# Optimization experiments

Hardware: AMD Instinct MI355X
Metric: run time of the kernel (lower is better)

## Reference

```python
import jax, jax.numpy as jnp
import numpy as np
import math

V, D, L, H, F, MAXLEN = 32000, 1024, 6, 16, 4096, 2048
B, S = 2, 2048
DK = D // H
EPS = 1e-5


def _ln(x, g, b):
    m = jnp.mean(x, axis=-1, keepdims=True)
    v = jnp.mean((x - m) ** 2, axis=-1, keepdims=True)
    return (x - m) / jnp.sqrt(v + EPS) * g + b


def setup_inputs() -> dict:
    key = jax.random.key(0)
    ks = jax.random.split(key, 12)
    std = 0.02
    inp = {
        "tokens": jax.random.randint(ks[0], (B, S), 0, V),
        "tok_emb": jax.random.normal(ks[1], (V, D), jnp.float32) * std,
        "pos_emb": jax.random.normal(ks[2], (MAXLEN, D), jnp.float32) * std,
        "Wq": jax.random.normal(ks[3], (L, D, D), jnp.float32) * std,
        "Wk": jax.random.normal(ks[4], (L, D, D), jnp.float32) * std,
        "Wv": jax.random.normal(ks[5], (L, D, D), jnp.float32) * std,
        "Wo": jax.random.normal(ks[6], (L, D, D), jnp.float32) * std,
        "ln1_g": jnp.ones((L, D), jnp.float32),
        "ln1_b": jnp.zeros((L, D), jnp.float32),
        "ln2_g": jnp.ones((L, D), jnp.float32),
        "ln2_b": jnp.zeros((L, D), jnp.float32),
        "W1": jax.random.normal(ks[7], (L, D, F), jnp.float32) * std,
        "b1": jnp.zeros((L, F), jnp.float32),
        "W2": jax.random.normal(ks[8], (L, F, D), jnp.float32) * std,
        "b2": jnp.zeros((L, D), jnp.float32),
        "lnf_g": jnp.ones((D,), jnp.float32),
        "lnf_b": jnp.zeros((D,), jnp.float32),
        "Wout": jax.random.normal(ks[9], (D, V), jnp.float32) * std,
    }
    return inp


def _block(x, Wq, Wk, Wv, Wo, ln1_g, ln1_b, ln2_g, ln2_b, W1, b1, W2, b2, mask):
    # causal multi-head attention (pre-LN)
    h = _ln(x, ln1_g, ln1_b)
    q = (h @ Wq).reshape(B, S, H, DK)
    k = (h @ Wk).reshape(B, S, H, DK)
    v = (h @ Wv).reshape(B, S, H, DK)
    scores = jnp.einsum("bqhd,bkhd->bhqk", q, k) / math.sqrt(DK)
    scores = jnp.where(mask, scores, -jnp.inf)
    attn = jax.nn.softmax(scores, axis=-1)
    ctx = jnp.einsum("bhqk,bkhd->bqhd", attn, v).reshape(B, S, D)
    x = x + ctx @ Wo
    # feed-forward
    h = _ln(x, ln2_g, ln2_b)
    h = jax.nn.gelu(h @ W1 + b1, approximate=False)
    x = x + h @ W2 + b2
    return x


def reference(tokens, tok_emb, pos_emb, Wq, Wk, Wv, Wo, ln1_g, ln1_b, ln2_g, ln2_b,
              W1, b1, W2, b2, lnf_g, lnf_b, Wout):
    x = tok_emb[tokens] + pos_emb[:S][None, :, :]  # [B,S,D]
    mask = jnp.tril(jnp.ones((S, S), bool))[None, None]  # [1,1,S,S]
    for l in range(L):
        x = _block(x, Wq[l], Wk[l], Wv[l], Wo[l], ln1_g[l], ln1_b[l],
                   ln2_g[l], ln2_b[l], W1[l], b1[l], W2[l], b2[l], mask)
    x = _ln(x, lnf_g, lnf_b)
    return x @ Wout  # [B,S,V] logits
```

## Files before the change

### kernel.cpp

```cpp
#include <hip/hip_runtime.h>
#include <stdint.h>

typedef unsigned short u16;
typedef __bf16 bf16x8 __attribute__((ext_vector_type(8)));
typedef u16   u16x8  __attribute__((ext_vector_type(8)));
typedef float f32x4  __attribute__((ext_vector_type(4)));

#define AS1(p) (const __attribute__((address_space(1))) void*)(p)
#define AS3(p) (__attribute__((address_space(3))) void*)(p)

__device__ __forceinline__ u16 f2b(float f){
  uint32_t u = __builtin_bit_cast(uint32_t, f);
  u = (u + 0x7FFFu + ((u >> 16) & 1u)) >> 16;
  return (u16)u;
}
__device__ __forceinline__ float fexp2(float x){
#if __has_builtin(__builtin_amdgcn_exp2f)
  return __builtin_amdgcn_exp2f(x);
#else
  return exp2f(x);
#endif
}

__global__ __launch_bounds__(256) void embed_k(const int* __restrict__ tokens,
                                               const float* __restrict__ te,
                                               const float* __restrict__ pe,
                                               float* __restrict__ x){
  const int n = blockIdx.x, tid = threadIdx.x;
  const int tok = tokens[n];
  float4 a = *(const float4*)&te[(size_t)tok * 1024 + tid * 4];
  const float4 p = *(const float4*)&pe[(size_t)(n & 2047) * 1024 + tid * 4];
  a.x += p.x; a.y += p.y; a.z += p.z; a.w += p.w;
  *(float4*)&x[(size_t)n * 1024 + tid * 4] = a;
}

__global__ __launch_bounds__(256) void ln_k(const float* __restrict__ x,
                                            const float* __restrict__ g,
                                            const float* __restrict__ b,
                                            u16* __restrict__ h){
  const int row = blockIdx.x, tid = threadIdx.x;
  const float4 v = *(const float4*)&x[(size_t)row * 1024 + tid * 4];
  float s = v.x + v.y + v.z + v.w;
  float q = v.x*v.x + v.y*v.y + v.z*v.z + v.w*v.w;
#pragma unroll
  for (int m = 32; m; m >>= 1){ s += __shfl_xor(s, m); q += __shfl_xor(q, m); }
  __shared__ float ss[4], qq[4];
  if ((tid & 63) == 0){ ss[tid >> 6] = s; qq[tid >> 6] = q; }
  __syncthreads();
  s = ss[0] + ss[1] + ss[2] + ss[3];
  q = qq[0] + qq[1] + qq[2] + qq[3];
  const float mean = s * (1.f/1024.f);
  const float var  = q * (1.f/1024.f) - mean*mean;
  const float rstd = rsqrtf(var + 1e-5f);
  const float4 gv = *(const float4*)&g[tid*4];
  const float4 bv = *(const float4*)&b[tid*4];
  ushort4 o;
  o.x = f2b((v.x-mean)*rstd*gv.x + bv.x);
  o.y = f2b((v.y-mean)*rstd*gv.y + bv.y);
  o.z = f2b((v.z-mean)*rstd*gv.z + bv.z);
  o.w = f2b((v.w-mean)*rstd*gv.w + bv.w);
  *(ushort4*)&h[(size_t)row * 1024 + tid * 4] = o;
}

__device__ __forceinline__ void conv_tile(const float* __restrict__ src,
                                          u16* __restrict__ dst,
                                          int R, int C, int bx, int by,
                                          u16 (*t)[72], int tid){
  const int r0 = by * 64, c0 = bx * 64;
  const int row = tid >> 4, col4 = tid & 15;
#pragma unroll
  for (int p = 0; p < 4; ++p){
    const int r = row + p * 16;
    const float4 v = *(const float4*)&src[(size_t)(r0 + r) * C + c0 + col4 * 4];
    t[r][col4*4+0] = f2b(v.x); t[r][col4*4+1] = f2b(v.y);
    t[r][col4*4+2] = f2b(v.z); t[r][col4*4+3] = f2b(v.w);
  }
  __syncthreads();
#pragma unroll
  for (int p = 0; p < 4; ++p){
    const int rr = row + p * 16;
    ushort4 w;
    w.x = t[col4*4+0][rr]; w.y = t[col4*4+1][rr];
    w.z = t[col4*4+2][rr]; w.w = t[col4*4+3][rr];
    *(ushort4*)&dst[(size_t)(c0 + rr) * R + r0 + col4 * 4] = w;
  }
}

__global__ __launch_bounds__(256) void conv_t(const float* __restrict__ src,
                                              u16* __restrict__ dst,
                                              int R, int C){
  __shared__ u16 t[64][72];
  conv_tile(src, dst, R, C, blockIdx.x, blockIdx.y, t, threadIdx.x);
}

__global__ __launch_bounds__(256) void conv6_k(const float* __restrict__ Wq,
                                               const float* __restrict__ Wk,
                                               const float* __restrict__ Wv,
                                               const float* __restrict__ Wo,
                                               const float* __restrict__ W1,
                                               const float* __restrict__ W2,
                                               u16* __restrict__ qkvT,
                                               u16* __restrict__ woT,
                                               u16* __restrict__ w1T,
                                               u16* __restrict__ w2T){
  __shared__ u16 t[64][72];
  const int id = blockIdx.x;
  const float* src; u16* dst; int R, C, bx, by;
  if (id < 1024){
    R = 1024; C = 1024;
    const int m = id >> 8, tt = id & 255; bx = tt & 15; by = tt >> 4;
    if (m == 0){ src = Wq; dst = qkvT; }
    else if (m == 1){ src = Wk; dst = qkvT + 1048576; }
    else if (m == 2){ src = Wv; dst = qkvT + 2097152; }
    else { src = Wo; dst = woT; }
  } else if (id < 2048){
    const int tt = id - 1024; R = 1024; C = 4096; bx = tt & 63; by = tt >> 6;
    src = W1; dst = w1T;
  } else {
    const int tt = id - 2048; R = 4096; C = 1024; bx = tt & 15; by = tt >> 4;
    src = W2; dst = w2T;
  }
  conv_tile(src, dst, R, C, bx, by, t, threadIdx.x);
}

template<int EPI>
__global__ __launch_bounds__(256) void gemm_bt(const u16* __restrict__ A,
                                               const u16* __restrict__ BT,
                                               void* __restrict__ Cout,
                                               const float* __restrict__ bias,
                                               int M, int N, int K){
  __shared__ __attribute__((aligned(16))) u16 As[128 * 64];
  __shared__ __attribute__((aligned(16))) u16 Bs[128 * 64];
  const int tid = threadIdx.x;
  const int lane = tid & 63, wave = tid >> 6;
  const int m0 = blockIdx.x * 128, n0 = blockIdx.y * 128;
  const int wm = wave >> 1, wn = wave & 1;
  const int l15 = lane & 15, l4 = lane >> 4;

  const int srow = tid >> 3;
  const int skb  = ((tid & 7) ^ (srow & 7)) * 8;
  const u16* Ag = A  + (size_t)(m0 + srow) * K + skb;
  const u16* Bg = BT + (size_t)(n0 + srow) * K + skb;
  char* AsB = (char*)As + wave * 1024;
  char* BsB = (char*)Bs + wave * 1024;

  f32x4 acc[4][4] = {};

  for (int k0 = 0; k0 < K; k0 += 64){
    __syncthreads();
#pragma unroll
    for (int c = 0; c < 4; ++c){
      __builtin_amdgcn_global_load_lds(AS1(Ag + (size_t)(c*32)*K + k0), AS3(AsB + c*4096), 16, 0, 0);
      __builtin_amdgcn_global_load_lds(AS1(Bg + (size_t)(c*32)*K + k0), AS3(BsB + c*4096), 16, 0, 0);
    }
    __syncthreads();
#pragma unroll
    for (int kk = 0; kk < 64; kk += 32){
      const int krd = kk + l4 * 8;
      const int kx  = (lane & 7) * 8;
      bf16x8 af[4], bfv[4];
#pragma unroll
      for (int mi = 0; mi < 4; ++mi){
        const int r = wm*64 + mi*16 + l15;
        af[mi] = *(const bf16x8*)&As[r*64 + (krd ^ kx)];
      }
#pragma unroll
      for (int ni = 0; ni < 4; ++ni){
        const int r = wn*64 + ni*16 + l15;
        bfv[ni] = *(const bf16x8*)&Bs[r*64 + (krd ^ kx)];
      }
#pragma unroll
      for (int mi = 0; mi < 4; ++mi)
#pragma unroll
        for (int ni = 0; ni < 4; ++ni)
          acc[mi][ni] = __builtin_amdgcn_mfma_f32_16x16x32_bf16(af[mi], bfv[ni], acc[mi][ni], 0, 0, 0);
    }
  }

#pragma unroll
  for (int mi = 0; mi < 4; ++mi){
    const int r = m0 + wm*64 + mi*16 + l4*4;
#pragma unroll
    for (int ni = 0; ni < 4; ++ni){
      const int c = n0 + wn*64 + ni*16 + l15;
      const f32x4 a = acc[mi][ni];
      if constexpr (EPI == 0){
        u16* C = (u16*)Cout;
#pragma unroll
        for (int j = 0; j < 4; ++j) C[(size_t)(r+j)*N + c] = f2b(a[j]);
      } else if constexpr (EPI == 1){
        float* C = (float*)Cout;
        const float bb = bias ? bias[c] : 0.f;
#pragma unroll
        for (int j = 0; j < 4; ++j){ const size_t o = (size_t)(r+j)*N + c; C[o] += a[j] + bb; }
      } else if constexpr (EPI == 2){
        u16* C = (u16*)Cout;
        const float bb = bias[c];
#pragma unroll
        for (int j = 0; j < 4; ++j){
          const float xv = a[j] + bb;
          C[(size_t)(r+j)*N + c] = f2b(0.5f * xv * (1.f + erff(xv * 0.70710678118654752f)));
        }
      } else {
        float* C = (float*)Cout;
#pragma unroll
        for (int j = 0; j < 4; ++j) C[(size_t)(r+j)*N + c] = a[j];
      }
    }
  }
}

template<int EPI>
__global__ __launch_bounds__(512) void gemm_bt2(const u16* __restrict__ A,
                                                const u16* __restrict__ BT,
                                                void* __restrict__ Cout,
                                                const float* __restrict__ bias,
                                                int M, int N, int K){
  __shared__ __attribute__((aligned(16))) u16 Ls[3][2][256*32];
  const int tid = threadIdx.x;
  const int lane = tid & 63, wave = tid >> 6;
  const int m0 = blockIdx.x * 256, n0 = blockIdx.y * 256;
  const int wm = wave >> 2, wn = wave & 3;
  const int l15 = lane & 15, l4 = lane >> 4;

  const int su  = (lane >> 3) & 7;
  const int c8  = (lane & 7) ^ su;
  const int rloc= ((lane >> 3) << 1) | (c8 >> 2);
  const int xl  = (c8 & 3) * 8;

  const u16* Asrc = A  + (size_t)(m0 + wave*16 + rloc) * K + xl;
  const u16* Bsrc = BT + (size_t)(n0 + wave*16 + rloc) * K + xl;
  char* lds0 = (char*)&Ls[0][0][0];
  const int wb = wave * 1024;

#define LOFF(r) (((r) >> 1)*64 + (((((((r) & 1) << 2) | l4)) ^ (((r) >> 1) & 7))*8))

#define STG(sb, k0, L) do{ \
    __builtin_amdgcn_global_load_lds(AS1(Asrc + (size_t)((L)*128)*K + (size_t)(k0)), \
        AS3(lds0 + (sb)*32768 +         (L)*8192 + wb), 16, 0, 0); \
    __builtin_amdgcn_global_load_lds(AS1(Bsrc + (size_t)((L)*128)*K + (size_t)(k0)), \
        AS3(lds0 + (sb)*32768 + 16384 + (L)*8192 + wb), 16, 0, 0); \
  }while(0)

#define MM(mi, a) do{ \
    acc[mi][0] = __builtin_amdgcn_mfma_f32_16x16x32_bf16((a), bf[0], acc[mi][0], 0, 0, 0); \
    acc[mi][1] = __builtin_amdgcn_mfma_f32_16x16x32_bf16((a), bf[1], acc[mi][1], 0, 0, 0); \
    acc[mi][2] = __builtin_amdgcn_mfma_f32_16x16x32_bf16((a), bf[2], acc[mi][2], 0, 0, 0); \
    acc[mi][3] = __builtin_amdgcn_mfma_f32_16x16x32_bf16((a), bf[3], acc[mi][3], 0, 0, 0); \
  }while(0)

  f32x4 acc[8][4] = {};
  const int nt = K >> 5;

  STG(0, 0, 0);  STG(0, 0, 1);
  STG(1, 32, 0); STG(1, 32, 1);
  asm volatile("s_waitcnt vmcnt(4)" ::: "memory");
  __builtin_amdgcn_s_barrier();

  int buf = 0;
  for (int t = 0; t < nt; ++t){
    const u16* LA = &Ls[buf][0][0];
    const u16* LB = &Ls[buf][1][0];
    int sb = buf + 2; if (sb >= 3) sb -= 3;
    const int kn = (t + 2) << 5;
    const bool st = (t + 2) < nt;

    bf16x8 bf[4], af0, af1;
#pragma unroll
    for (int ni = 0; ni < 4; ++ni)
      bf[ni] = *(const bf16x8*)&LB[LOFF(wn*64 + ni*16 + l15)];
    af0 = *(const bf16x8*)&LA[LOFF(wm*128 + 0*16 + l15)];
    af1 = *(const bf16x8*)&LA[LOFF(wm*128 + 1*16 + l15)];
    if (st) STG(sb, kn, 0);
    __builtin_amdgcn_s_barrier();
    __builtin_amdgcn_s_setprio(1);
    MM(0, af0); MM(1, af1);
    __builtin_amdgcn_s_setprio(0);

    af0 = *(const bf16x8*)&LA[LOFF(wm*128 + 2*16 + l15)];
    af1 = *(const bf16x8*)&LA[LOFF(wm*128 + 3*16 + l15)];
    __builtin_amdgcn_s_barrier();
    __builtin_amdgcn_s_setprio(1);
    MM(2, af0); MM(3, af1);
    __builtin_amdgcn_s_setprio(0);

    af0 = *(const bf16x8*)&LA[LOFF(wm*128 + 4*16 + l15)];
    af1 = *(const bf16x8*)&LA[LOFF(wm*128 + 5*16 + l15)];
    if (st) STG(sb, kn, 1);
    __builtin_amdgcn_s_barrier();
    __builtin_amdgcn_s_setprio(1);
    MM(4, af0); MM(5, af1);
    __builtin_amdgcn_s_setprio(0);

    af0 = *(const bf16x8*)&LA[LOFF(wm*128 + 6*16 + l15)];
    af1 = *(const bf16x8*)&LA[LOFF(wm*128 + 7*16 + l15)];
    __builtin_amdgcn_s_barrier();
    __builtin_amdgcn_s_setprio(1);
    MM(6, af0); MM(7, af1);
    __builtin_amdgcn_s_setprio(0);

    if (t < nt - 2){
      asm volatile("s_waitcnt vmcnt(4)" ::: "memory");
      __builtin_amdgcn_s_barrier();
    } else if (t == nt - 2){
      asm volatile("s_waitcnt vmcnt(0)" ::: "memory");
      __builtin_amdgcn_s_barrier();
    }
    buf = buf + 1; if (buf >= 3) buf -= 3;
  }
#undef STG
#undef LOFF
#undef MM

#pragma unroll
  for (int mi = 0; mi < 8; ++mi){
    const int r = m0 + wm*128 + mi*16 + l4*4;
#pragma unroll
    for (int ni = 0; ni < 4; ++ni){
      const int c = n0 + wn*64 + ni*16 + l15;
      const f32x4 a = acc[mi][ni];
      if constexpr (EPI == 0){
        u16* C = (u16*)Cout;
#pragma unroll
        for (int j = 0; j < 4; ++j) C[(size_t)(r+j)*N + c] = f2b(a[j]);
      } else if constexpr (EPI == 2){
        u16* C = (u16*)Cout;
        const float bb = bias[c];
#pragma unroll
        for (int j = 0; j < 4; ++j){
          const float xv = a[j] + bb;
          C[(size_t)(r+j)*N + c] = f2b(0.5f * xv * (1.f + erff(xv * 0.70710678118654752f)));
        }
      } else {
        float* C = (float*)Cout;
#pragma unroll
        for (int j = 0; j < 4; ++j) C[(size_t)(r+j)*N + c] = a[j];
      }
    }
  }
}

__global__ __launch_bounds__(256) void attn_k(const u16* __restrict__ qkv,
                                              u16* __restrict__ ctx){
  __shared__ __attribute__((aligned(16))) u16 Ks[2][64*64];
  __shared__ __attribute__((aligned(16))) u16 Vt[2][64][72];
  __shared__ __attribute__((aligned(16))) u16 Ps[8][16][72];
  const int tid = threadIdx.x, lane = tid & 63, w = tid >> 6;
  const int l15 = lane & 15, l4 = lane >> 4;
  const int b = blockIdx.y >> 4, h = blockIdx.y & 15;
  const int bx = gridDim.x - 1 - blockIdx.x;
  const int q0 = bx * 128;
  const int qw = q0 + w * 32;
  const u16* qb = qkv + (size_t)b * 2048 * 3072 + h * 64;
  const u16* kb = qb + 1024;
  const u16* vb = qb + 2048;

  const bf16x8 qa0 = *(const bf16x8*)&qb[(size_t)(qw + l15) * 3072 + l4 * 8];
  const bf16x8 qa1 = *(const bf16x8*)&qb[(size_t)(qw + l15) * 3072 + 32 + l4 * 8];
  const bf16x8 qb0 = *(const bf16x8*)&qb[(size_t)(qw + 16 + l15) * 3072 + l4 * 8];
  const bf16x8 qb1 = *(const bf16x8*)&qb[(size_t)(qw + 16 + l15) * 3072 + 32 + l4 * 8];

  f32x4 oa[4] = {}, ob[4] = {};
  float mra = -__builtin_inff(), lra = 0.f;
  float mrb = -__builtin_inff(), lrb = 0.f;
  const float CEXP = 0.18033688f;

  const int T = 2*bx + 2;
  const int vd = tid & 63, vkc = w;

  {
    u16* kd = &Ks[0][0];
#pragma unroll
    for (int s = 0; s < 2; ++s){
      const int r = s*32 + w*8 + (lane >> 3);
      __builtin_amdgcn_global_load_lds(AS1(kb + (size_t)r * 3072 + ((lane & 7) ^ (r & 7)) * 8),
                                       AS3(kd + (s*32 + w*8) * 64), 16, 0, 0);
    }
    u16 vr[16];
#pragma unroll
    for (int i = 0; i < 16; ++i) vr[i] = vb[(size_t)(vkc*16 + i) * 3072 + vd];
    u16x8 va, vb2;
#pragma unroll
    for (int i = 0; i < 8; ++i){ va[i] = vr[i]; vb2[i] = vr[8+i]; }
    *(u16x8*)&Vt[0][vd][vkc*16]     = va;
    *(u16x8*)&Vt[0][vd][vkc*16 + 8] = vb2;
  }
  __syncthreads();

  for (int t = 0; t < T; ++t){
    const int cur = t & 1;
    const int kt = t * 64;

    u16 vr[16];
    if (t + 1 < T){
      const int ktn = kt + 64;
      u16* kd = &Ks[cur ^ 1][0];
#pragma unroll
      for (int s = 0; s < 2; ++s){
        const int r = s*32 + w*8 + (lane >> 3);
        __builtin_amdgcn_global_load_lds(AS1(kb + (size_t)(ktn + r) * 3072 + ((lane & 7) ^ (r & 7)) * 8),
                                         AS3(kd + (s*32 + w*8) * 64), 16, 0, 0);
      }
#pragma unroll
      for (int i = 0; i < 16; ++i) vr[i] = vb[(size_t)(ktn + vkc*16 + i) * 3072 + vd];
    }

    if (kt <= qw + 31){
      f32x4 sta[4] = {}, stb[4] = {};
      __builtin_amdgcn_s_setprio(1);
#pragma unroll
      for (int t4 = 0; t4 < 4; ++t4){
        const int r = t4*16 + l15;
        const int sx = l15 & 7;
        const bf16x8 kf0 = *(const bf16x8*)&Ks[cur][r*64 + ((l4       ^ sx) * 8)];
        const bf16x8 kf1 = *(const bf16x8*)&Ks[cur][r*64 + (((4 + l4) ^ sx) * 8)];
        sta[t4] = __builtin_amdgcn_mfma_f32_16x16x32_bf16(kf0, qa0, sta[t4], 0, 0, 0);
        sta[t4] = __builtin_amdgcn_mfma_f32_16x16x32_bf16(kf1, qa1, sta[t4], 0, 0, 0);
        stb[t4] = __builtin_amdgcn_mfma_f32_16x16x32_bf16(kf0, qb0, stb[t4], 0, 0, 0);
        stb[t4] = __builtin_amdgcn_mfma_f32_16x16x32_bf16(kf1, qb1, stb[t4], 0, 0, 0);
      }
      __builtin_amdgcn_s_setprio(0);

      bf16x8 pa0, pa1, pb0, pb1;
      {
        float sv[16];
#pragma unroll
        for (int t4 = 0; t4 < 4; ++t4)
#pragma unroll
          for (int j = 0; j < 4; ++j) sv[t4*4 + j] = sta[t4][j];
        if (kt + 63 > qw){
          const int qrow = qw + l15;
#pragma unroll
          for (int t4 = 0; t4 < 4; ++t4)
#pragma unroll
            for (int j = 0; j < 4; ++j){
              const int k = kt + t4*16 + l4*4 + j;
              if (k > qrow) sv[t4*4 + j] = -__builtin_inff();
            }
        }
        float x0 = fmaxf(fmaxf(sv[0],  sv[1]),  sv[2]);
        float x1 = fmaxf(fmaxf(sv[3],  sv[4]),  sv[5]);
        float x2 = fmaxf(fmaxf(sv[6],  sv[7]),  sv[8]);
        float x3 = fmaxf(fmaxf(sv[9],  sv[10]), sv[11]);
        float x4 = fmaxf(fmaxf(sv[12], sv[13]), sv[14]);
        float mt = fmaxf(fmaxf(fmaxf(x0, x1), x2), fmaxf(fmaxf(x3, x4), sv[15]));
        mt = fmaxf(mt, __shfl_xor(mt, 16));
        mt = fmaxf(mt, __shfl_xor(mt, 32));
        if (__any(mt > mra + 64.f)){
          const float mn = fmaxf(mra, mt);
          const float sc = fexp2((mra - mn) * CEXP);
          lra *= sc;
          mra = mn;
#pragma unroll
          for (int j = 0; j < 4; ++j){
            const float scj = __shfl(sc, l4*4 + j);
            oa[0][j] *= scj; oa[1][j] *= scj; oa[2][j] *= scj; oa[3][j] *= scj;
          }
        }
        const float mb = -mra * CEXP;
#pragma unroll
        for (int i = 0; i < 16; ++i) sv[i] = fexp2(__builtin_fmaf(sv[i], CEXP, mb));
        {
          float s0 = sv[0]+sv[1], s1 = sv[2]+sv[3], s2 = sv[4]+sv[5], s3 = sv[6]+sv[7];
          float s4 = sv[8]+sv[9], s5 = sv[10]+sv[11], s6 = sv[12]+sv[13], s7 = sv[14]+sv[15];
          float rs = (s0+s1) + (s2+s3) + ((s4+s5) + (s6+s7));
          rs += __shfl_xor(rs, 16);
          rs += __shfl_xor(rs, 32);
          lra += rs;
        }
#pragma unroll
        for (int t4 = 0; t4 < 4; ++t4){
          uint32_t pk0, pk1;
          asm("v_cvt_pk_bf16_f32 %0, %1, %2" : "=v"(pk0) : "v"(sv[t4*4+0]), "v"(sv[t4*4+1]));
          asm("v_cvt_pk_bf16_f32 %0, %1, %2" : "=v"(pk1) : "v"(sv[t4*4+2]), "v"(sv[t4*4+3]));
          *(uint32_t*)&Ps[2*w][l15][t4*16 + l4*4]     = pk0;
          *(uint32_t*)&Ps[2*w][l15][t4*16 + l4*4 + 2] = pk1;
        }
        pa0 = *(const bf16x8*)&Ps[2*w][l15][l4*8];
        pa1 = *(const bf16x8*)&Ps[2*w][l15][32 + l4*8];
      }
      {
        float sv[16];
#pragma unroll
        for (int t4 = 0; t4 < 4; ++t4)
#pragma unroll
          for (int j = 0; j < 4; ++j) sv[t4*4 + j] = stb[t4][j];
        if (kt + 63 > qw + 16){
          const int qrow = qw + 16 + l15;
#pragma unroll
          for (int t4 = 0; t4 < 4; ++t4)
#pragma unroll
            for (int j = 0; j < 4; ++j){
              const int k = kt + t4*16 + l4*4 + j;
              if (k > qrow) sv[t4*4 + j] = -__builtin_inff();
            }
        }
        float x0 = fmaxf(fmaxf(sv[0],  sv[1]),  sv[2]);
        float x1 = fmaxf(fmaxf(sv[3],  sv[4]),  sv[5]);
        float x2 = fmaxf(fmaxf(sv[6],  sv[7]),  sv[8]);
        float x3 = fmaxf(fmaxf(sv[9],  sv[10]), sv[11]);
        float x4 = fmaxf(fmaxf(sv[12], sv[13]), sv[14]);
        float mt = fmaxf(fmaxf(fmaxf(x0, x1), x2), fmaxf(fmaxf(x3, x4), sv[15]));
        mt = fmaxf(mt, __shfl_xor(mt, 16));
        mt = fmaxf(mt, __shfl_xor(mt, 32));
        if (__any(mt > mrb + 64.f)){
          const float mn = fmaxf(mrb, mt);
          const float sc = fexp2((mrb - mn) * CEXP);
          lrb *= sc;
          mrb = mn;
#pragma unroll
          for (int j = 0; j < 4; ++j){
            const float scj = __shfl(sc, l4*4 + j);
            ob[0][j] *= scj; ob[1][j] *= scj; ob[2][j] *= scj; ob[3][j] *= scj;
          }
        }
        const float mb = -mrb * CEXP;
#pragma unroll
        for (int i = 0; i < 16; ++i) sv[i] = fexp2(__builtin_fmaf(sv[i], CEXP, mb));
        {
          float s0 = sv[0]+sv[1], s1 = sv[2]+sv[3], s2 = sv[4]+sv[5], s3 = sv[6]+sv[7];
          float s4 = sv[8]+sv[9], s5 = sv[10]+sv[11], s6 = sv[12]+sv[13], s7 = sv[14]+sv[15];
          float rs = (s0+s1) + (s2+s3) + ((s4+s5) + (s6+s7));
          rs += __shfl_xor(rs, 16);
          rs += __shfl_xor(rs, 32);
          lrb += rs;
        }
#pragma unroll
        for (int t4 = 0; t4 < 4; ++t4){
          uint32_t pk0, pk1;
          asm("v_cvt_pk_bf16_f32 %0, %1, %2" : "=v"(pk0) : "v"(sv[t4*4+0]), "v"(sv[t4*4+1]));
          asm("v_cvt_pk_bf16_f32 %0, %1, %2" : "=v"(pk1) : "v"(sv[t4*4+2]), "v"(sv[t4*4+3]));
          *(uint32_t*)&Ps[2*w+1][l15][t4*16 + l4*4]     = pk0;
          *(uint32_t*)&Ps[2*w+1][l15][t4*16 + l4*4 + 2] = pk1;
        }
        pb0 = *(const bf16x8*)&Ps[2*w+1][l15][l4*8];
        pb1 = *(const bf16x8*)&Ps[2*w+1][l15][32 + l4*8];
      }

      __builtin_amdgcn_s_setprio(1);
#pragma unroll
      for (int dt = 0; dt < 4; ++dt){
        const bf16x8 vf0 = *(const bf16x8*)&Vt[cur][dt*16 + l15][l4*8];
        const bf16x8 vf1 = *(const bf16x8*)&Vt[cur][dt*16 + l15][32 + l4*8];
        oa[dt] = __builtin_amdgcn_mfma_f32_16x16x32_bf16(pa0, vf0, oa[dt], 0, 0, 0);
        oa[dt] = __builtin_amdgcn_mfma_f32_16x16x32_bf16(pa1, vf1, oa[dt], 0, 0, 0);
        ob[dt] = __builtin_amdgcn_mfma_f32_16x16x32_bf16(pb0, vf0, ob[dt], 0, 0, 0);
        ob[dt] = __builtin_amdgcn_mfma_f32_16x16x32_bf16(pb1, vf1, ob[dt], 0, 0, 0);
      }
      __builtin_amdgcn_s_setprio(0);
    }

    if (t + 1 < T){
      u16x8 va, vb2;
#pragma unroll
      for (int i = 0; i < 8; ++i){ va[i] = vr[i]; vb2[i] = vr[8+i]; }
      *(u16x8*)&Vt[cur ^ 1][vd][vkc*16]     = va;
      *(u16x8*)&Vt[cur ^ 1][vd][vkc*16 + 8] = vb2;
    }
    __syncthreads();
  }

  const float inva = 1.f / lra, invb = 1.f / lrb;
#pragma unroll
  for (int j = 0; j < 4; ++j){
    const float ia = __shfl(inva, l4*4 + j);
    const float ib = __shfl(invb, l4*4 + j);
    u16* ca = ctx + (size_t)b * 2048 * 1024 + (size_t)(qw + l4*4 + j) * 1024 + h * 64;
    u16* cb2 = ca + (size_t)16 * 1024;
#pragma unroll
    for (int dt = 0; dt < 4; ++dt){
      ca[dt*16 + l15]  = f2b(oa[dt][j] * ia);
      cb2[dt*16 + l15] = f2b(ob[dt][j] * ib);
    }
  }
}

extern "C" void kernel_launch(void* const* d_in, const int* in_sizes, int n_in,
                              void* d_out, int out_size, void* d_ws, size_t ws_size,
                              hipStream_t stream){
  const int*   tokens = (const int*)d_in[0];
  const float* tok_emb= (const float*)d_in[1];
  const float* pos_emb= (const float*)d_in[2];
  const float* Wq  = (const float*)d_in[3];
  const float* Wk  = (const float*)d_in[4];
  const float* Wv  = (const float*)d_in[5];
  const float* Wo  = (const float*)d_in[6];
  const float* ln1g= (const float*)d_in[7];
  const float* ln1b= (const float*)d_in[8];
  const float* ln2g= (const float*)d_in[9];
  const float* ln2b= (const float*)d_in[10];
  const float* W1  = (const float*)d_in[11];
  const float* b1  = (const float*)d_in[12];
  const float* W2  = (const float*)d_in[13];
  const float* b2  = (const float*)d_in[14];
  const float* lnfg= (const float*)d_in[15];
  const float* lnfb= (const float*)d_in[16];
  const float* Wout= (const float*)d_in[17];

  char* ws = (char*)d_ws;
  float* x    = (float*)(ws + 0);
  u16*   h    = (u16*)(ws + 16777216);
  u16*   qkv  = (u16*)(ws + 25165824);
  u16*   ctxb = (u16*)(ws + 50331648);
  u16*   h1   = (u16*)(ws + 58720256);
  u16*   wT   = (u16*)(ws + 92274688);
  u16*   wqkvT= wT;
  u16*   woT  = wT + (size_t)3072 * 1024;
  u16*   w1T  = woT + (size_t)1024 * 1024;
  u16*   w2T  = w1T + (size_t)4096 * 1024;
  u16*   woutT= wT;

  embed_k<<<4096, 256, 0, stream>>>(tokens, tok_emb, pos_emb, x);

  for (int l = 0; l < 6; ++l){
    conv6_k<<<3072, 256, 0, stream>>>(Wq + (size_t)l*1048576, Wk + (size_t)l*1048576,
                                      Wv + (size_t)l*1048576, Wo + (size_t)l*1048576,
                                      W1 + (size_t)l*4194304, W2 + (size_t)l*4194304,
                                      wqkvT, woT, w1T, w2T);

    ln_k<<<4096, 256, 0, stream>>>(x, ln1g + l*1024, ln1b + l*1024, h);
    gemm_bt2<0><<<dim3(16,12), 512, 0, stream>>>(h, wqkvT, qkv, nullptr, 4096, 3072, 1024);
    attn_k<<<dim3(16,32), 256, 0, stream>>>(qkv, ctxb);
    gemm_bt<1><<<dim3(32,8), 256, 0, stream>>>(ctxb, woT, x, nullptr, 4096, 1024, 1024);
    ln_k<<<4096, 256, 0, stream>>>(x, ln2g + l*1024, ln2b + l*1024, h);
    gemm_bt2<2><<<dim3(16,16), 512, 0, stream>>>(h, w1T, h1, b1 + l*4096, 4096, 4096, 1024);
    gemm_bt<1><<<dim3(32,8), 256, 0, stream>>>(h1, w2T, x, b2 + l*1024, 4096, 1024, 4096);
  }

  ln_k<<<4096, 256, 0, stream>>>(x, lnfg, lnfb, h);
  conv_t<<<dim3(500,16), 256, 0, stream>>>(Wout, woutT, 1024, 32000);
  gemm_bt2<3><<<dim3(16,125), 512, 0, stream>>>(h, woutT, (float*)d_out, nullptr, 4096, 32000, 1024);
}
```

Measured before the change: 2.248 ms.

## Triple-buffer GEMM LDS tiles with async prefetch interleaved into MFMA phases

Rewrites the gemm_bt main loop to use a three-stage LDS ring of 32-wide K tiles. Global-to-LDS loads for tile t+2 are issued in two halves between MFMA phases, and vmcnt waits replace the full __syncthreads pairs, so loads overlap with compute. Each K tile is split into two MFMA phases with s_setprio around them, and a new XOR swizzle layout is used for the LDS tiles. The cost is more barriers per K step, a hand-tuned wait count, and tighter correctness dependencies on the async load ordering.

```diff
diff --git a/kernel.cpp b/kernel.cpp
--- a/kernel.cpp
+++ b/kernel.cpp
@@ -129,53 +129,87 @@
                                                void* __restrict__ Cout,
                                                const float* __restrict__ bias,
                                                int M, int N, int K){
-  __shared__ __attribute__((aligned(16))) u16 As[128 * 64];
-  __shared__ __attribute__((aligned(16))) u16 Bs[128 * 64];
+  __shared__ __attribute__((aligned(16))) u16 Ls[3][2][128*32];
   const int tid = threadIdx.x;
   const int lane = tid & 63, wave = tid >> 6;
   const int m0 = blockIdx.x * 128, n0 = blockIdx.y * 128;
   const int wm = wave >> 1, wn = wave & 1;
   const int l15 = lane & 15, l4 = lane >> 4;
 
-  const int srow = tid >> 3;
-  const int skb  = ((tid & 7) ^ (srow & 7)) * 8;
-  const u16* Ag = A  + (size_t)(m0 + srow) * K + skb;
-  const u16* Bg = BT + (size_t)(n0 + srow) * K + skb;
-  char* AsB = (char*)As + wave * 1024;
-  char* BsB = (char*)Bs + wave * 1024;
+  const int su  = (lane >> 3) & 7;
+  const int c8  = (lane & 7) ^ su;
+  const int rloc= ((lane >> 3) << 1) | (c8 >> 2);
+  const int xl  = (c8 & 3) * 8;
+
+  const u16* Asrc = A  + (size_t)(m0 + wave*16 + rloc) * K + xl;
+  const u16* Bsrc = BT + (size_t)(n0 + wave*16 + rloc) * K + xl;
+  char* lds0 = (char*)&Ls[0][0][0];
+  const int wb = wave * 1024;
+
+#define LOFF(r) (((r) >> 1)*64 + (((((((r) & 1) << 2) | l4)) ^ (((r) >> 1) & 7))*8))
+
+#define STG(sb, k0, L) do{ \
+    __builtin_amdgcn_global_load_lds(AS1(Asrc + (size_t)((L)*64)*K + (size_t)(k0)), \
+        AS3(lds0 + (sb)*16384 +        (L)*4096 + wb), 16, 0, 0); \
+    __builtin_amdgcn_global_load_lds(AS1(Bsrc + (size_t)((L)*64)*K + (size_t)(k0)), \
+        AS3(lds0 + (sb)*16384 + 8192 + (L)*4096 + wb), 16, 0, 0); \
+  }while(0)
 
   f32x4 acc[4][4] = {};
-
-  for (int k0 = 0; k0 < K; k0 += 64){
-    __syncthreads();
-#pragma unroll
-    for (int c = 0; c < 4; ++c){
-      __builtin_amdgcn_global_load_lds(AS1(Ag + (size_t)(c*32)*K + k0), AS3(AsB + c*4096), 16, 0, 0);
-      __builtin_amdgcn_global_load_lds(AS1(Bg + (size_t)(c*32)*K + k0), AS3(BsB + c*4096), 16, 0, 0);
-    }
-    __syncthreads();
-#pragma unroll
-    for (int kk = 0; kk < 64; kk += 32){
-      const int krd = kk + l4 * 8;
-      const int kx  = (lane & 7) * 8;
-      bf16x8 af[4], bfv[4];
-#pragma unroll
-      for (int mi = 0; mi < 4; ++mi){
-        const int r = wm*64 + mi*16 + l15;
-        af[mi] = *(const bf16x8*)&As[r*64 + (krd ^ kx)];
-      }
-#pragma unroll
-      for (int ni = 0; ni < 4; ++ni){
-        const int r = wn*64 + ni*16 + l15;
-        bfv[ni] = *(const bf16x8*)&Bs[r*64 + (krd ^ kx)];
-      }
-#pragma unroll
-      for (int mi = 0; mi < 4; ++mi)
-#pragma unroll
-        for (int ni = 0; ni < 4; ++ni)
-          acc[mi][ni] = __builtin_amdgcn_mfma_f32_16x16x32_bf16(af[mi], bfv[ni], acc[mi][ni], 0, 0, 0);
-    }
-  }
+  const int nt = K >> 5;
+
+  STG(0, 0, 0);  STG(0, 0, 1);
+  STG(1, 32, 0); STG(1, 32, 1);
+  asm volatile("s_waitcnt vmcnt(4)" ::: "memory");
+  __builtin_amdgcn_s_barrier();
+
+  int buf = 0;
+  for (int t = 0; t < nt; ++t){
+    const u16* LA = &Ls[buf][0][0];
+    const u16* LB = &Ls[buf][1][0];
+    int sb = buf + 2; if (sb >= 3) sb -= 3;
+    const int kn = (t + 2) << 5;
+    const bool st = (t + 2) < nt;
+
+    bf16x8 bfv[4], a0, a1;
+#pragma unroll
+    for (int ni = 0; ni < 4; ++ni)
+      bfv[ni] = *(const bf16x8*)&LB[LOFF(wn*64 + ni*16 + l15)];
+    a0 = *(const bf16x8*)&LA[LOFF(wm*64 + 0*16 + l15)];
+    a1 = *(const bf16x8*)&LA[LOFF(wm*64 + 1*16 + l15)];
+    if (st) STG(sb, kn, 0);
+    __builtin_amdgcn_s_barrier();
+    __builtin_amdgcn_s_setprio(1);
+#pragma unroll
+    for (int ni = 0; ni < 4; ++ni){
+      acc[0][ni] = __builtin_amdgcn_mfma_f32_16x16x32_bf16(a0, bfv[ni], acc[0][ni], 0, 0, 0);
+      acc[1][ni] = __builtin_amdgcn_mfma_f32_16x16x32_bf16(a1, bfv[ni], acc[1][ni], 0, 0, 0);
+    }
+    __builtin_amdgcn_s_setprio(0);
+
+    a0 = *(const bf16x8*)&LA[LOFF(wm*64 + 2*16 + l15)];
+    a1 = *(const bf16x8*)&LA[LOFF(wm*64 + 3*16 + l15)];
+    if (st) STG(sb, kn, 1);
+    __builtin_amdgcn_s_barrier();
+    __builtin_amdgcn_s_setprio(1);
+#pragma unroll
+    for (int ni = 0; ni < 4; ++ni){
+      acc[2][ni] = __builtin_amdgcn_mfma_f32_16x16x32_bf16(a0, bfv[ni], acc[2][ni], 0, 0, 0);
+      acc[3][ni] = __builtin_amdgcn_mfma_f32_16x16x32_bf16(a1, bfv[ni], acc[3][ni], 0, 0, 0);
+    }
+    __builtin_amdgcn_s_setprio(0);
+
+    if (t < nt - 2){
+      asm volatile("s_waitcnt vmcnt(4)" ::: "memory");
+      __builtin_amdgcn_s_barrier();
+    } else if (t == nt - 2){
+      asm volatile("s_waitcnt vmcnt(0)" ::: "memory");
+      __builtin_amdgcn_s_barrier();
+    }
+    buf = buf + 1; if (buf >= 3) buf -= 3;
+  }
+#undef STG
+#undef LOFF
 
 #pragma unroll
   for (int mi = 0; mi < 4; ++mi){
```

Result: faster. 2.057 ms (-8.5%).
